# Kernel tuning notes

Measured on AMD Instinct MI355X. Metric: run time of the kernel, lower is better.

The kernel has to match this reference:

```python
import jax, jax.numpy as jnp
import numpy as np

EPS = 1e-6


def gaussian_filt(x, k, sigma):
    # x: [B,H,W,C]; depthwise gaussian conv with reflect padding, matching
    # TCFormer guassian_filt (kernel uses analytic 1/(2*pi*var) normalization).
    C = x.shape[-1]
    coords = jnp.arange(k, dtype=x.dtype)
    mean = (k - 1) / 2.0
    var = float(sigma) ** 2
    g1 = jnp.exp(-(coords - mean) ** 2 / (2.0 * var))
    gk = (g1[:, None] * g1[None, :]) / (2.0 * np.pi * var)  # [k,k]
    w = jnp.tile(gk[:, :, None, None], (1, 1, 1, C))  # HWIO, depthwise
    pad = (k - 1) // 2
    xp = jnp.pad(x, ((0, 0), (pad, pad), (pad, pad), (0, 0)), mode='reflect')
    return jax.lax.conv_general_dilated(
        xp, w, (1, 1), 'VALID',
        dimension_numbers=('NHWC', 'HWIO', 'NHWC'), feature_group_count=C)


def token2map(x, loc, H, W, kernel_size, sigma):
    # Scatter-mean tokens x [B,N,C] at normalized locations loc [B,N,2] in [-1,1]
    # onto an HxW grid, then gaussian-splat to fill holes. Returns NHWC map.
    B, N, C = x.shape
    loc = jnp.clip(loc, -1.0, 1.0)
    px = jnp.clip(jnp.round(0.5 * (loc[..., 0] + 1.0) * W - 0.5).astype(jnp.int32), 0, W - 1)
    py = jnp.clip(jnp.round(0.5 * (loc[..., 1] + 1.0) * H - 0.5).astype(jnp.int32), 0, H - 1)
    idx = py * W + px + jnp.arange(B, dtype=jnp.int32)[:, None] * (H * W)  # [B,N]
    src = jnp.concatenate([x, jnp.ones((B, N, 1), x.dtype)], axis=-1)  # [B,N,C+1]
    out = jnp.zeros((B * H * W, C + 1), x.dtype).at[idx.reshape(-1)].add(src.reshape(-1, C + 1))
    out = out.reshape(B, H, W, C + 1)
    feat, cnt = out[..., :C], out[..., C:]
    feat = feat / (cnt + EPS)
    mask = (cnt > 0).astype(x.dtype)
    feat = feat * mask
    if kernel_size > 1:
        # reconstruct_feature: fill empty cells with gaussian-interpolated values
        y = gaussian_filt(jnp.concatenate([feat, mask], axis=-1), kernel_size, sigma)
        fi, mi = y[..., :C], y[..., C:]
        fi = fi / (mi + EPS)
        fi = fi * (mi > 0).astype(x.dtype)
        feat = feat + (1.0 - mask) * fi
    return feat  # [B,H,W,C]


def layernorm(x, g, b, eps=1e-5):
    m = jnp.mean(x, axis=-1, keepdims=True)
    v = jnp.var(x, axis=-1, keepdims=True)
    return (x - m) / jnp.sqrt(v + eps) * g + b


def setup_inputs() -> dict:
    key = jax.random.key(0)
    ks = jax.random.split(key, 8)
    B, N, C, H, W = 8, 16384, 64, 128, 128
    SR = 8
    std = 0.02
    return {
        'x': jax.random.normal(ks[0], (B, N, C), jnp.float32),
        'x_source': jax.random.normal(ks[1], (B, N, C), jnp.float32),
        'loc_source': jax.random.uniform(ks[2], (B, N, 2), jnp.float32) * 2.0 - 1.0,
        'conf_source': jax.random.normal(ks[3], (B, N, 1), jnp.float32) * 0.1,
        'q_w': jax.random.normal(ks[4], (C, C), jnp.float32) * std,
        'kv_w': jax.random.normal(ks[5], (2 * C, C), jnp.float32) * std,
        'sr_w': jax.random.normal(ks[6], (SR, SR, C, C), jnp.float32) * np.sqrt(2.0 / (SR * SR * C)),
        'sr_b': jnp.zeros((C,), jnp.float32),
        'norm_w': jnp.ones((C,), jnp.float32),
        'norm_b': jnp.zeros((C,), jnp.float32),
        'proj_w': jax.random.normal(ks[7], (C, C), jnp.float32) * std,
        'proj_b': jnp.zeros((C,), jnp.float32),
        'H': H,
        'W': W,
    }


def reference(x, x_source, loc_source, conf_source, q_w, kv_w, sr_w, sr_b,
              norm_w, norm_b, proj_w, proj_b, H, W):
    B, N, C = x.shape
    num_heads = 1  # PVT stage-1
    hd = C // num_heads
    scale = hd ** -0.5
    sr = sr_w.shape[0]  # sr_ratio = 8

    # q projection: [B, nh, N, hd]
    q = (x @ q_w.T).reshape(B, N, num_heads, hd).transpose(0, 2, 1, 3)

    # token2map scatter-splat (kernel = sr_ratio + 1, sigma = 2)
    feat = token2map(x_source, loc_source, H, W, sr + 1, 2.0)  # [B,H,W,C]

    # SR conv (k = stride = sr_ratio), then layernorm
    xs = jax.lax.conv_general_dilated(
        feat, sr_w, (sr, sr), 'VALID',
        dimension_numbers=('NHWC', 'HWIO', 'NHWC')) + sr_b
    h, w = H // sr, W // sr
    xs = layernorm(xs.reshape(B, h * w, C), norm_w, norm_b)  # [B,M,C]

    # confidence map on the reduced grid (kernel_size=1 => pure scatter-mean)
    conf = token2map(conf_source, loc_source, h, w, 1, 1.0).reshape(B, h * w)  # [B,M]

    kv = (xs @ kv_w.T).reshape(B, h * w, 2, num_heads, hd)
    k = kv[:, :, 0].transpose(0, 2, 1, 3)  # [B,nh,M,hd]
    v = kv[:, :, 1].transpose(0, 2, 1, 3)

    attn = jnp.einsum('bhnd,bhmd->bhnm', q, k) * scale
    attn = attn + conf[:, None, None, :]  # additive confidence bias
    attn = jax.nn.softmax(attn, axis=-1)
    out = jnp.einsum('bhnm,bhmd->bhnd', attn, v)
    out = out.transpose(0, 2, 1, 3).reshape(B, N, C)
    return out @ proj_w.T + proj_b
```

## Files before the change

### kernel.cpp

```cpp
#include <hip/hip_runtime.h>
#include <hip/hip_bf16.h>

#define NN 16384
#define NC 64
#define GH 128
#define GW 128
#define GM 256

typedef __attribute__((ext_vector_type(8))) short bf16x8;
typedef __attribute__((ext_vector_type(4))) float f32x4;

static __device__ __forceinline__ int reflect128(int i){
  if (i < 0) i = -i;
  if (i > 127) i = 254 - i;
  return i;
}

static __device__ __forceinline__ ushort f2bf(float f){
  union { float f; unsigned u; } v; v.f = f;
  unsigned r = v.u + 0x7fffu + ((v.u >> 16) & 1u);
  return (ushort)(r >> 16);
}

static __device__ __forceinline__ int cell_of(float l, float S2, int hi){
  l = fminf(fmaxf(l, -1.f), 1.f);
  float u = l + 1.f;
  int p = (int)rintf(u*S2 - 0.5f);
  return min(max(p,0),hi);
}

__global__ __launch_bounds__(256) void k_scatter_feat(
    const float* __restrict__ xsrc, const float* __restrict__ loc,
    float* __restrict__ featg){
  int gid = blockIdx.x*256 + threadIdx.x;
  int t = gid >> 6;
  int b = t >> 14;
  int px = cell_of(loc[2*t],   64.f, 127);
  int py = cell_of(loc[2*t+1], 64.f, 127);
  int cell = (b*GH + py)*GW + px;
  atomicAdd(&featg[cell*NC + (gid & 63)], xsrc[gid]);
}

__global__ __launch_bounds__(256) void k_scatter_aux(
    const float* __restrict__ loc, const float* __restrict__ csrc,
    float* __restrict__ cnt, float* __restrict__ csum, float* __restrict__ ccnt){
  int t = blockIdx.x*256 + threadIdx.x;
  int b = t >> 14;
  int px = cell_of(loc[2*t],   64.f, 127);
  int py = cell_of(loc[2*t+1], 64.f, 127);
  atomicAdd(&cnt[(b*GH+py)*GW+px], 1.0f);
  int qx = cell_of(loc[2*t],   8.f, 15);
  int qy = cell_of(loc[2*t+1], 8.f, 15);
  int cell = b*GM + qy*16 + qx;
  atomicAdd(&csum[cell], csrc[t]);
  atomicAdd(&ccnt[cell], 1.0f);
}

__global__ __launch_bounds__(256) void k_finalize_feat(
    float* __restrict__ featg, const float* __restrict__ cnt){
  int gid = blockIdx.x*256 + threadIdx.x;
  float cn = cnt[gid>>6];
  float v  = featg[gid];
  featg[gid] = (cn > 0.f) ? v/(cn+1e-6f) : 0.f;
}

__global__ __launch_bounds__(256) void k_finalize_conf(
    const float* __restrict__ csum, const float* __restrict__ ccnt,
    float* __restrict__ conf){
  int i = blockIdx.x*256 + threadIdx.x;
  float cn = ccnt[i];
  conf[i] = (cn > 0.f) ? csum[i]/(cn+1e-6f) : 0.f;
}

__global__ __launch_bounds__(256) void k_fill2(
    const float* __restrict__ cnt, float* __restrict__ feat){
  int gid = blockIdx.x*256 + threadIdx.x;
  int p = gid >> 2, cg = gid & 3;
  if (cnt[p] > 0.f) return;
  int b = p>>14, py=(p>>7)&127, px=p&127;
  const float fn = 0.039788735772973836f;
  float g1[9];
  #pragma unroll
  for (int i=0;i<9;++i){ float d=(float)i-4.f; g1[i]=__expf(-d*d*0.125f); }
  float4 acc[4];
  #pragma unroll
  for (int i=0;i<4;++i) acc[i]=make_float4(0.f,0.f,0.f,0.f);
  float msum=0.f;
  for (int dy=0; dy<9; ++dy){
    int iy = reflect128(py-4+dy);
    for (int dx=0; dx<9; ++dx){
      int ix = reflect128(px-4+dx);
      int q  = (b*GH+iy)*GW+ix;
      if (cnt[q] <= 0.f) continue;
      float wn = g1[dy]*g1[dx]*fn;
      msum += wn;
      const float4* fr = (const float4*)&feat[q*NC + cg*16];
      #pragma unroll
      for (int k=0;k<4;++k){
        float4 vv = fr[k];
        acc[k].x += wn*vv.x; acc[k].y += wn*vv.y;
        acc[k].z += wn*vv.z; acc[k].w += wn*vv.w;
      }
    }
  }
  if (msum <= 0.f) return;
  float inv = 1.f/(msum + 1e-6f);
  float4* o = (float4*)&feat[p*NC + cg*16];
  #pragma unroll
  for (int k=0;k<4;++k)
    o[k] = make_float4(acc[k].x*inv, acc[k].y*inv, acc[k].z*inv, acc[k].w*inv);
}

static __device__ __forceinline__ int rowswz(int bid){
  return ((bid & 7) << 7) + (bid >> 3);
}

__global__ __launch_bounds__(256) void k_finfillh(
    float* __restrict__ feat, const float* __restrict__ cnt,
    float* __restrict__ feath, float* __restrict__ maskh){
  __shared__ float F[GW*NC];
  __shared__ float CR[GW];
  int py = rowswz(blockIdx.x), t = threadIdx.x;
  const float fn = 0.039788735772973836f;
  float g1n[9];
  #pragma unroll
  for (int i=0;i<9;++i){ float d=(float)i-4.f; g1n[i]=__expf(-d*d*0.125f)*fn; }
  if (t < GW) CR[t] = cnt[py*GW + t];
  __syncthreads();
  for (int i=t*4; i<GW*NC; i+=1024){
    int px = i>>6;
    float cn = CR[px];
    float inv = (cn > 0.f) ? 1.f/(cn+1e-6f) : 0.f;
    float4 v = *(const float4*)&feat[(size_t)py*GW*NC + i];
    v.x*=inv; v.y*=inv; v.z*=inv; v.w*=inv;
    *(float4*)&F[i] = v;
    *(float4*)&feat[(size_t)py*GW*NC + i] = v;
  }
  __syncthreads();
  for (int i=t*4; i<GW*NC; i+=1024){
    int px = i>>6, c = i&63;
    float4 acc = make_float4(0.f,0.f,0.f,0.f);
    #pragma unroll
    for (int dx=0; dx<9; ++dx){
      int ix = reflect128(px-4+dx);
      float w = g1n[dx];
      float4 v = *(const float4*)&F[ix*NC + c];
      acc.x += w*v.x; acc.y += w*v.y; acc.z += w*v.z; acc.w += w*v.w;
    }
    *(float4*)&feath[(size_t)py*GW*NC + i] = acc;
  }
  if (t < GW){
    float hm = 0.f;
    #pragma unroll
    for (int dx=0; dx<9; ++dx){
      int ix = reflect128(t-4+dx);
      hm += g1n[dx]*((CR[ix] > 0.f) ? 1.f : 0.f);
    }
    maskh[py*GW + t] = hm;
  }
}

__global__ __launch_bounds__(256) void k_fillv(
    float* __restrict__ feat, const float* __restrict__ cnt,
    const float* __restrict__ feath, const float* __restrict__ maskh){
  int pyg = rowswz(blockIdx.x), t = threadIdx.x;
  int b = pyg >> 7, pyl = pyg & 127;
  int px = t>>1, c0 = (t&1)<<5;
  float g1[9];
  #pragma unroll
  for (int i=0;i<9;++i){ float d=(float)i-4.f; g1[i]=__expf(-d*d*0.125f); }
  float cn = cnt[pyg*GW + px];
  float ym = 0.f;
  int ry[9];
  #pragma unroll
  for (int dy=0; dy<9; ++dy){
    ry[dy] = b*GH + reflect128(pyl-4+dy);
    ym += g1[dy]*maskh[ry[dy]*GW + px];
  }
  if (cn > 0.f || ym <= 0.f) return;
  float inv = 1.f/(ym + 1e-6f);
  float4 acc[8];
  #pragma unroll
  for (int k=0;k<8;++k) acc[k]=make_float4(0.f,0.f,0.f,0.f);
  #pragma unroll
  for (int dy=0; dy<9; ++dy){
    float w = g1[dy];
    const float4* hf = (const float4*)&feath[((size_t)ry[dy]*GW+px)*NC + c0];
    #pragma unroll
    for (int k=0;k<8;++k){
      float4 v = hf[k];
      acc[k].x += w*v.x; acc[k].y += w*v.y; acc[k].z += w*v.z; acc[k].w += w*v.w;
    }
  }
  float4* o = (float4*)&feat[((size_t)pyg*GW+px)*NC + c0];
  #pragma unroll
  for (int k=0;k<8;++k)
    o[k] = make_float4(acc[k].x*inv, acc[k].y*inv, acc[k].z*inv, acc[k].w*inv);
}

__global__ __launch_bounds__(256) void k_srconv(
    const float* __restrict__ feat, const float* __restrict__ srw,
    float* __restrict__ xs0){
  alignas(16) __shared__ float A[64*65];
  alignas(16) __shared__ float Bs[64*64];
  int mt = blockIdx.x, kh = blockIdx.y;
  int t = threadIdx.x;
  int tm = t>>4, tn = t&15;
  float acc[4][4] = {{0.f}};
  for (int kc=0; kc<8; ++kc){
    __syncthreads();
    for (int idx=t; idx<4096; idx+=256){
      int mr = idx>>6, kk = idx&63;
      int m = mt*64+mr;
      int b = m>>8, oh=(m>>4)&15, ow=m&15;
      A[mr*65+kk] = feat[(((b*GH)+(oh*8+kh))*GW + ow*8)*NC + kc*64 + kk];
    }
    for (int idx=t; idx<4096; idx+=256)
      Bs[idx] = srw[(kh*512 + kc*64)*64 + idx];
    __syncthreads();
    for (int kk=0; kk<64; ++kk){
      float4 bv = *(const float4*)&Bs[kk*64 + tn*4];
      #pragma unroll
      for (int i=0;i<4;++i){
        float av = A[(tm*4+i)*65 + kk];
        acc[i][0] += av*bv.x; acc[i][1] += av*bv.y;
        acc[i][2] += av*bv.z; acc[i][3] += av*bv.w;
      }
    }
  }
  #pragma unroll
  for (int i=0;i<4;++i)
    #pragma unroll
    for (int j=0;j<4;++j)
      atomicAdd(&xs0[(mt*64+tm*4+i)*64 + tn*4+j], acc[i][j]);
}

__global__ __launch_bounds__(256) void k_srconv2(
    const float* __restrict__ feat, const float* __restrict__ srw,
    float* __restrict__ part){
  alignas(16) __shared__ float A[64*65];
  alignas(16) __shared__ float Bs[64*64];
  int mt = blockIdx.x, kh = blockIdx.y, kq = blockIdx.z;
  int t = threadIdx.x;
  int tm = t>>4, tn = t&15;
  float acc[4][4] = {{0.f}};
  for (int kc=0; kc<4; ++kc){
    int kw = kq*4 + kc;
    __syncthreads();
    for (int idx=t; idx<4096; idx+=256){
      int mr = idx>>6, kk = idx&63;
      int m = mt*64+mr;
      int b = m>>8, oh=(m>>4)&15, ow=m&15;
      A[mr*65+kk] = feat[(((b*GH)+(oh*8+kh))*GW + ow*8 + kw)*NC + kk];
    }
    for (int idx=t; idx<4096; idx+=256)
      Bs[idx] = srw[(kh*512 + kw*64)*64 + idx];
    __syncthreads();
    for (int kk=0; kk<64; ++kk){
      float4 bv = *(const float4*)&Bs[kk*64 + tn*4];
      #pragma unroll
      for (int i=0;i<4;++i){
        float av = A[(tm*4+i)*65 + kk];
        acc[i][0] += av*bv.x; acc[i][1] += av*bv.y;
        acc[i][2] += av*bv.z; acc[i][3] += av*bv.w;
      }
    }
  }
  float* pdst = part + (size_t)(kh*2+kq)*2048*64;
  #pragma unroll
  for (int i=0;i<4;++i)
    #pragma unroll
    for (int j=0;j<4;++j)
      pdst[(mt*64+tm*4+i)*64 + tn*4+j] = acc[i][j];
}

__global__ __launch_bounds__(256) void k_ln(
    const float* __restrict__ xs0, const float* __restrict__ srb,
    const float* __restrict__ nw, const float* __restrict__ nbv,
    float* __restrict__ xs){
  int row  = blockIdx.x*4 + (threadIdx.x>>6);
  int lane = threadIdx.x & 63;
  float v = xs0[row*64+lane] + srb[lane];
  float s = v;
  #pragma unroll
  for (int off=32; off; off>>=1) s += __shfl_xor(s, off, 64);
  float mean = s*(1.f/64.f);
  float d = v - mean;
  float s2 = d*d;
  #pragma unroll
  for (int off=32; off; off>>=1) s2 += __shfl_xor(s2, off, 64);
  float var = s2*(1.f/64.f);
  xs[row*64+lane] = d*(1.f/sqrtf(var+1e-5f))*nw[lane] + nbv[lane];
}

__global__ __launch_bounds__(256) void k_ln16(
    const float* __restrict__ part, const float* __restrict__ srb,
    const float* __restrict__ nw, const float* __restrict__ nbv,
    float* __restrict__ xs){
  int row  = blockIdx.x*4 + (threadIdx.x>>6);
  int lane = threadIdx.x & 63;
  float v = srb[lane];
  #pragma unroll
  for (int ps=0; ps<16; ++ps)
    v += part[(size_t)ps*2048*64 + row*64 + lane];
  float s = v;
  #pragma unroll
  for (int off=32; off; off>>=1) s += __shfl_xor(s, off, 64);
  float mean = s*(1.f/64.f);
  float d = v - mean;
  float s2 = d*d;
  #pragma unroll
  for (int off=32; off; off>>=1) s2 += __shfl_xor(s2, off, 64);
  float var = s2*(1.f/64.f);
  xs[row*64+lane] = d*(1.f/sqrtf(var+1e-5f))*nw[lane] + nbv[lane];
}

__global__ __launch_bounds__(256) void k_kv1(
    const float* __restrict__ xs, const float* __restrict__ kvw,
    float* __restrict__ kraw, float* __restrict__ vraw){
  int gid = blockIdx.x*256 + threadIdx.x;
  int r = gid >> 6, d = gid & 63;
  const float* xr = &xs[r*64];
  float ka=0.f, va=0.f;
  for (int c=0;c<64;++c){
    float xc = xr[c];
    ka += xc*kvw[d*64+c];
    va += xc*kvw[(64+d)*64+c];
  }
  kraw[gid] = ka;
  vraw[gid] = va;
}

__global__ __launch_bounds__(256) void k_kvproj2(
    const float* __restrict__ kraw, const float* __restrict__ vraw,
    const float* __restrict__ qw, const float* __restrict__ pw,
    ushort* __restrict__ KB, ushort* __restrict__ VB){
  int gid = blockIdx.x*256 + threadIdx.x;
  int r = gid >> 6, c = gid & 63;
  int b = r >> 8, m = r & 255;
  const float* kr = &kraw[r*64];
  const float* vr = &vraw[r*64];
  float ak=0.f, av=0.f;
  for (int i=0;i<64;++i){
    ak += kr[i]*qw[i*64+c];
    av += vr[i]*pw[c*64+i];
  }
  {
    int nt = m>>4, l15 = m&15, kb = c>>5, h = (c>>3)&3, j = c&7;
    KB[((((b*16 + nt)*2 + kb)*4 + h)*16 + l15)*8 + j] = f2bf(ak);
  }
  {
    int ct = c>>4, n15 = c&15, kb2 = m>>5, h2 = (m>>3)&3, j2 = m&7;
    VB[((((b*4 + ct)*8 + kb2)*4 + h2)*16 + n15)*8 + j2] = f2bf(av);
  }
}

__global__ __launch_bounds__(256) void k_attn5(
    const float* __restrict__ x, const ushort* __restrict__ KB,
    const ushort* __restrict__ VB, const float* __restrict__ conf,
    const float* __restrict__ projb, float* __restrict__ out){
  alignas(16) __shared__ ushort P[4*4096];
  int t = threadIdx.x, w = t>>6, l = t&63;
  int b = blockIdx.x >> 8;
  int row0 = ((blockIdx.x & 255) << 6) + (w<<4);
  int l15 = l & 15, h = l >> 4;
  const ushort* KBb = KB + b*16384;
  const ushort* VBb = VB + b*16384;

  bf16x8 xa[2];
  {
    const float* xr = x + (size_t)(b*NN + row0 + l15)*64 + h*8;
    #pragma unroll
    for (int kb=0; kb<2; ++kb){
      float4 a0 = *(const float4*)(xr + 32*kb);
      float4 a1 = *(const float4*)(xr + 32*kb + 4);
      bf16x8 v;
      v[0]=(short)f2bf(a0.x); v[1]=(short)f2bf(a0.y);
      v[2]=(short)f2bf(a0.z); v[3]=(short)f2bf(a0.w);
      v[4]=(short)f2bf(a1.x); v[5]=(short)f2bf(a1.y);
      v[6]=(short)f2bf(a1.z); v[7]=(short)f2bf(a1.w);
      xa[kb]=v;
    }
  }

  f32x4 acc[16];
  #pragma unroll
  for (int nt=0;nt<16;++nt) acc[nt] = (f32x4){0.f,0.f,0.f,0.f};
  #pragma unroll
  for (int nt=0;nt<16;++nt){
    bf16x8 b0 = *(const bf16x8*)(KBb + (nt*2+0)*512 + l*8);
    bf16x8 b1 = *(const bf16x8*)(KBb + (nt*2+1)*512 + l*8);
    acc[nt] = __builtin_amdgcn_mfma_f32_16x16x32_bf16(xa[0], b0, acc[nt], 0,0,0);
    acc[nt] = __builtin_amdgcn_mfma_f32_16x16x32_bf16(xa[1], b1, acc[nt], 0,0,0);
  }

  float rs[4] = {0.f,0.f,0.f,0.f};
  ushort* Pw = P + w*4096;
  #pragma unroll
  for (int nt=0;nt<16;++nt){
    float cf = conf[b*GM + nt*16 + l15];
    #pragma unroll
    for (int reg=0;reg<4;++reg){
      float p = __expf(fmaf(acc[nt][reg], 0.125f, cf));
      rs[reg] += p;
      int m   = nt*16 + l15;
      int row = h*4 + reg;
      int ld  = ((m>>3)&3)*16 + row;
      int idx = ((m>>5)*512 + ld*8 + (m&7)) ^ (ld & 0x38);
      Pw[idx] = f2bf(p);
    }
  }
  #pragma unroll
  for (int off=1; off<16; off<<=1){
    #pragma unroll
    for (int reg=0;reg<4;++reg) rs[reg] += __shfl_xor(rs[reg], off, 64);
  }

  f32x4 oacc[4];
  #pragma unroll
  for (int ct=0;ct<4;++ct) oacc[ct] = (f32x4){0.f,0.f,0.f,0.f};
  #pragma unroll
  for (int kb2=0;kb2<8;++kb2){
    int ridx = (kb2*512 + l*8) ^ (l & 0x38);
    bf16x8 pa = *(const bf16x8*)(Pw + ridx);
    #pragma unroll
    for (int ct=0;ct<4;++ct){
      bf16x8 vb = *(const bf16x8*)(VBb + (ct*8+kb2)*512 + l*8);
      oacc[ct] = __builtin_amdgcn_mfma_f32_16x16x32_bf16(pa, vb, oacc[ct], 0,0,0);
    }
  }

  float* OT = (float*)Pw;
  #pragma unroll
  for (int ct=0;ct<4;++ct){
    float pb4 = projb[ct*16 + l15];
    #pragma unroll
    for (int reg=0;reg<4;++reg)
      OT[(h*4+reg)*68 + ct*16 + l15] = oacc[ct][reg]/rs[reg] + pb4;
  }
  #pragma unroll
  for (int i=0;i<4;++i){
    int row = i*4 + h;
    float4 v = *(const float4*)&OT[row*68 + l15*4];
    *(float4*)&out[(size_t)(b*NN + row0 + row)*64 + l15*4] = v;
  }
}

extern "C" void kernel_launch(void* const* d_in, const int* in_sizes, int n_in,
                              void* d_out, int out_size, void* d_ws, size_t ws_size,
                              hipStream_t stream){
  const float* x    = (const float*)d_in[0];
  const float* xsrc = (const float*)d_in[1];
  const float* loc  = (const float*)d_in[2];
  const float* csrc = (const float*)d_in[3];
  const float* qw   = (const float*)d_in[4];
  const float* kvw  = (const float*)d_in[5];
  const float* srw  = (const float*)d_in[6];
  const float* srb  = (const float*)d_in[7];
  const float* nw   = (const float*)d_in[8];
  const float* nbv  = (const float*)d_in[9];
  const float* pw   = (const float*)d_in[10];
  const float* pb   = (const float*)d_in[11];
  float* out = (float*)d_out;
  float* ws = (float*)d_ws;

  size_t of_feat  = 0;
  size_t of_cnt   = of_feat  + 8ull*GH*GW*NC;
  size_t of_csum  = of_cnt   + 8ull*GH*GW;
  size_t of_ccnt  = of_csum  + 8ull*GM;
  size_t zero_end = of_ccnt  + 8ull*GM;
  size_t of_feath = zero_end;
  size_t of_maskh = of_feath + 8ull*GH*GW*NC;
  size_t of_part  = of_maskh + 8ull*GH*GW;
  size_t of_conf  = of_part  + 16ull*2048*64;
  size_t of_xs    = of_conf  + 8ull*GM;
  size_t of_kr    = of_xs    + 8ull*GM*NC;
  size_t of_vr    = of_kr    + 8ull*GM*NC;
  size_t of_kb    = of_vr    + 8ull*GM*NC;
  size_t of_vb    = of_kb    + 8ull*8192;
  size_t total_p  = of_vb    + 8ull*8192;

  if (ws_size >= total_p*sizeof(float)){
    hipMemsetAsync(ws, 0, zero_end*sizeof(float), stream);
    k_scatter_feat <<<8*NN*NC/256, 256, 0, stream>>>(xsrc, loc, ws+of_feat);
    k_scatter_aux  <<<8*NN/256,    256, 0, stream>>>(loc, csrc, ws+of_cnt, ws+of_csum, ws+of_ccnt);
    k_finalize_conf<<<8*GM/256,    256, 0, stream>>>(ws+of_csum, ws+of_ccnt, ws+of_conf);
    k_finfillh     <<<8*GH,        256, 0, stream>>>(ws+of_feat, ws+of_cnt, ws+of_feath, ws+of_maskh);
    k_fillv        <<<8*GH,        256, 0, stream>>>(ws+of_feat, ws+of_cnt, ws+of_feath, ws+of_maskh);
    dim3 gconv(32, 8, 2);
    k_srconv2      <<<gconv,       256, 0, stream>>>(ws+of_feat, srw, ws+of_part);
    k_ln16         <<<8*GM/4,      256, 0, stream>>>(ws+of_part, srb, nw, nbv, ws+of_xs);
    k_kv1          <<<8*GM*NC/256, 256, 0, stream>>>(ws+of_xs, kvw, ws+of_kr, ws+of_vr);
    k_kvproj2      <<<8*GM*NC/256, 256, 0, stream>>>(ws+of_kr, ws+of_vr, qw, pw,
                                                     (ushort*)(ws+of_kb), (ushort*)(ws+of_vb));
    k_attn5        <<<8*NN/64,     256, 0, stream>>>(x, (const ushort*)(ws+of_kb),
                                                     (const ushort*)(ws+of_vb),
                                                     ws+of_conf, pb, out);
  } else {
    size_t f_feat = 0;
    size_t f_cnt  = f_feat + 8ull*GH*GW*NC;
    size_t f_csum = f_cnt  + 8ull*GH*GW;
    size_t f_ccnt = f_csum + 8ull*GM;
    size_t f_xs0  = f_ccnt + 8ull*GM;
    size_t f_zero = f_xs0  + 8ull*GM*NC;
    size_t f_conf = f_zero;
    size_t f_xs   = f_conf + 8ull*GM;
    size_t f_kr   = f_xs   + 8ull*GM*NC;
    size_t f_vr   = f_kr   + 8ull*GM*NC;
    size_t f_kb   = f_vr   + 8ull*GM*NC;
    size_t f_vb   = f_kb   + 8ull*8192;
    hipMemsetAsync(ws, 0, f_zero*sizeof(float), stream);
    k_scatter_feat <<<8*NN*NC/256, 256, 0, stream>>>(xsrc, loc, ws+f_feat);
    k_scatter_aux  <<<8*NN/256,    256, 0, stream>>>(loc, csrc, ws+f_cnt, ws+f_csum, ws+f_ccnt);
    k_finalize_feat<<<8*GH*GW*NC/256, 256, 0, stream>>>(ws+f_feat, ws+f_cnt);
    k_finalize_conf<<<8*GM/256,    256, 0, stream>>>(ws+f_csum, ws+f_ccnt, ws+f_conf);
    k_fill2        <<<8*GH*GW*4/256, 256, 0, stream>>>(ws+f_cnt, ws+f_feat);
    dim3 gconv(8*GM/64, 8);
    k_srconv       <<<gconv,       256, 0, stream>>>(ws+f_feat, srw, ws+f_xs0);
    k_ln           <<<8*GM/4,      256, 0, stream>>>(ws+f_xs0, srb, nw, nbv, ws+f_xs);
    k_kv1          <<<8*GM*NC/256, 256, 0, stream>>>(ws+f_xs, kvw, ws+f_kr, ws+f_vr);
    k_kvproj2      <<<8*GM*NC/256, 256, 0, stream>>>(ws+f_kr, ws+f_vr, qw, pw,
                                                     (ushort*)(ws+f_kb), (ushort*)(ws+f_vb));
    k_attn5        <<<8*NN/64,     256, 0, stream>>>(x, (const ushort*)(ws+f_kb),
                                                     (const ushort*)(ws+f_vb),
                                                     ws+f_conf, pb, out);
  }
}
```

Measured before the change: 206.6 us.

## Fuse layernorm and KV projections into one kernel; chunk attention softmax-PV loop

```diff
diff --git a/kernel.cpp b/kernel.cpp
--- a/kernel.cpp
+++ b/kernel.cpp
@@ -293,28 +293,6 @@
   xs[row*64+lane] = d*(1.f/sqrtf(var+1e-5f))*nw[lane] + nbv[lane];
 }
 
-__global__ __launch_bounds__(256) void k_ln16(
-    const float* __restrict__ part, const float* __restrict__ srb,
-    const float* __restrict__ nw, const float* __restrict__ nbv,
-    float* __restrict__ xs){
-  int row  = blockIdx.x*4 + (threadIdx.x>>6);
-  int lane = threadIdx.x & 63;
-  float v = srb[lane];
-  #pragma unroll
-  for (int ps=0; ps<16; ++ps)
-    v += part[(size_t)ps*2048*64 + row*64 + lane];
-  float s = v;
-  #pragma unroll
-  for (int off=32; off; off>>=1) s += __shfl_xor(s, off, 64);
-  float mean = s*(1.f/64.f);
-  float d = v - mean;
-  float s2 = d*d;
-  #pragma unroll
-  for (int off=32; off; off>>=1) s2 += __shfl_xor(s2, off, 64);
-  float var = s2*(1.f/64.f);
-  xs[row*64+lane] = d*(1.f/sqrtf(var+1e-5f))*nw[lane] + nbv[lane];
-}
-
 __global__ __launch_bounds__(256) void k_kv1(
     const float* __restrict__ xs, const float* __restrict__ kvw,
     float* __restrict__ kraw, float* __restrict__ vraw){
@@ -355,6 +333,56 @@
   }
 }
 
+__global__ __launch_bounds__(256) void k_kvfused(
+    const float* __restrict__ part, const float* __restrict__ srb,
+    const float* __restrict__ nw, const float* __restrict__ nbv,
+    const float* __restrict__ kvw, const float* __restrict__ qw,
+    const float* __restrict__ pw,
+    ushort* __restrict__ KB, ushort* __restrict__ VB){
+  __shared__ float XR[4][64], KR[4][64], VR[4][64];
+  int t = threadIdx.x;
+  int rl = t>>6, d = t&63;
+  int r  = blockIdx.x*4 + rl;
+  float v = srb[d];
+  #pragma unroll
+  for (int ps=0; ps<16; ++ps)
+    v += part[(size_t)ps*2048*64 + r*64 + d];
+  float s = v;
+  #pragma unroll
+  for (int off=32; off; off>>=1) s += __shfl_xor(s, off, 64);
+  float mean = s*(1.f/64.f);
+  float dd = v - mean;
+  float s2 = dd*dd;
+  #pragma unroll
+  for (int off=32; off; off>>=1) s2 += __shfl_xor(s2, off, 64);
+  float var = s2*(1.f/64.f);
+  XR[rl][d] = dd*(1.f/sqrtf(var+1e-5f))*nw[d] + nbv[d];
+  __syncthreads();
+  float ka=0.f, va=0.f;
+  for (int cc=0; cc<64; ++cc){
+    float xc = XR[rl][cc];
+    ka += xc*kvw[d*64+cc];
+    va += xc*kvw[(64+d)*64+cc];
+  }
+  KR[rl][d] = ka; VR[rl][d] = va;
+  __syncthreads();
+  int c = d;
+  float ak=0.f, av=0.f;
+  for (int i=0;i<64;++i){
+    ak += KR[rl][i]*qw[i*64+c];
+    av += VR[rl][i]*pw[c*64+i];
+  }
+  int b = r>>8, m = r&255;
+  {
+    int nt = m>>4, l15 = m&15, kb = c>>5, h = (c>>3)&3, j = c&7;
+    KB[((((b*16 + nt)*2 + kb)*4 + h)*16 + l15)*8 + j] = f2bf(ak);
+  }
+  {
+    int ct = c>>4, n15 = c&15, kb2 = m>>5, h2 = (m>>3)&3, j2 = m&7;
+    VB[((((b*4 + ct)*8 + kb2)*4 + h2)*16 + n15)*8 + j2] = f2bf(av);
+  }
+}
+
 __global__ __launch_bounds__(256) void k_attn5(
     const float* __restrict__ x, const ushort* __restrict__ KB,
     const ushort* __restrict__ VB, const float* __restrict__ conf,
@@ -366,7 +394,6 @@
   int l15 = l & 15, h = l >> 4;
   const ushort* KBb = KB + b*16384;
   const ushort* VBb = VB + b*16384;
-
   bf16x8 xa[2];
   {
     const float* xr = x + (size_t)(b*NN + row0 + l15)*64 + h*8;
@@ -382,7 +409,6 @@
       xa[kb]=v;
     }
   }
-
   f32x4 acc[16];
   #pragma unroll
   for (int nt=0;nt<16;++nt) acc[nt] = (f32x4){0.f,0.f,0.f,0.f};
@@ -393,7 +419,6 @@
     acc[nt] = __builtin_amdgcn_mfma_f32_16x16x32_bf16(xa[0], b0, acc[nt], 0,0,0);
     acc[nt] = __builtin_amdgcn_mfma_f32_16x16x32_bf16(xa[1], b1, acc[nt], 0,0,0);
   }
-
   float rs[4] = {0.f,0.f,0.f,0.f};
   ushort* Pw = P + w*4096;
   #pragma unroll
@@ -415,7 +440,6 @@
     #pragma unroll
     for (int reg=0;reg<4;++reg) rs[reg] += __shfl_xor(rs[reg], off, 64);
   }
-
   f32x4 oacc[4];
   #pragma unroll
   for (int ct=0;ct<4;++ct) oacc[ct] = (f32x4){0.f,0.f,0.f,0.f};
@@ -428,6 +452,102 @@
       bf16x8 vb = *(const bf16x8*)(VBb + (ct*8+kb2)*512 + l*8);
       oacc[ct] = __builtin_amdgcn_mfma_f32_16x16x32_bf16(pa, vb, oacc[ct], 0,0,0);
     }
+  }
+  float* OT = (float*)Pw;
+  #pragma unroll
+  for (int ct=0;ct<4;++ct){
+    float pb4 = projb[ct*16 + l15];
+    #pragma unroll
+    for (int reg=0;reg<4;++reg)
+      OT[(h*4+reg)*68 + ct*16 + l15] = oacc[ct][reg]/rs[reg] + pb4;
+  }
+  #pragma unroll
+  for (int i=0;i<4;++i){
+    int row = i*4 + h;
+    float4 v = *(const float4*)&OT[row*68 + l15*4];
+    *(float4*)&out[(size_t)(b*NN + row0 + row)*64 + l15*4] = v;
+  }
+}
+
+__global__ __launch_bounds__(256) void k_attn6(
+    const float* __restrict__ x, const ushort* __restrict__ KB,
+    const ushort* __restrict__ VB, const float* __restrict__ conf,
+    const float* __restrict__ projb, float* __restrict__ out){
+  alignas(16) __shared__ ushort P[4*4096];
+  int t = threadIdx.x, w = t>>6, l = t&63;
+  int b = blockIdx.x >> 8;
+  int row0 = ((blockIdx.x & 255) << 6) + (w<<4);
+  int l15 = l & 15, h = l >> 4;
+  const ushort* KBb = KB + b*16384;
+  const ushort* VBb = VB + b*16384;
+
+  bf16x8 xa[2];
+  {
+    const float* xr = x + (size_t)(b*NN + row0 + l15)*64 + h*8;
+    #pragma unroll
+    for (int kb=0; kb<2; ++kb){
+      float4 a0 = *(const float4*)(xr + 32*kb);
+      float4 a1 = *(const float4*)(xr + 32*kb + 4);
+      bf16x8 v;
+      v[0]=(short)f2bf(a0.x); v[1]=(short)f2bf(a0.y);
+      v[2]=(short)f2bf(a0.z); v[3]=(short)f2bf(a0.w);
+      v[4]=(short)f2bf(a1.x); v[5]=(short)f2bf(a1.y);
+      v[6]=(short)f2bf(a1.z); v[7]=(short)f2bf(a1.w);
+      xa[kb]=v;
+    }
+  }
+
+  float rs[4] = {0.f,0.f,0.f,0.f};
+  f32x4 oacc[4];
+  #pragma unroll
+  for (int ct=0;ct<4;++ct) oacc[ct] = (f32x4){0.f,0.f,0.f,0.f};
+  ushort* Pw = P + w*4096;
+
+  #pragma unroll
+  for (int c=0;c<4;++c){
+    f32x4 acc[4];
+    #pragma unroll
+    for (int q=0;q<4;++q) acc[q] = (f32x4){0.f,0.f,0.f,0.f};
+    #pragma unroll
+    for (int q=0;q<4;++q){
+      int nt = c*4 + q;
+      bf16x8 b0 = *(const bf16x8*)(KBb + (nt*2+0)*512 + l*8);
+      bf16x8 b1 = *(const bf16x8*)(KBb + (nt*2+1)*512 + l*8);
+      acc[q] = __builtin_amdgcn_mfma_f32_16x16x32_bf16(xa[0], b0, acc[q], 0,0,0);
+      acc[q] = __builtin_amdgcn_mfma_f32_16x16x32_bf16(xa[1], b1, acc[q], 0,0,0);
+    }
+    #pragma unroll
+    for (int q=0;q<4;++q){
+      int nt = c*4 + q;
+      float cf = conf[b*GM + nt*16 + l15];
+      #pragma unroll
+      for (int reg=0;reg<4;++reg){
+        float p = __expf(fmaf(acc[q][reg], 0.125f, cf));
+        rs[reg] += p;
+        int m   = nt*16 + l15;
+        int row = h*4 + reg;
+        int ld  = ((m>>3)&3)*16 + row;
+        int idx = ((m>>5)*512 + ld*8 + (m&7)) ^ (ld & 0x38);
+        Pw[idx] = f2bf(p);
+      }
+    }
+    #pragma unroll
+    for (int kk=0;kk<2;++kk){
+      int kb2 = c*2 + kk;
+      int ridx = (kb2*512 + l*8) ^ (l & 0x38);
+      bf16x8 pa = *(const bf16x8*)(Pw + ridx);
+      #pragma unroll
+      for (int ct=0;ct<4;++ct){
+        bf16x8 vb = *(const bf16x8*)(VBb + (ct*8+kb2)*512 + l*8);
+        oacc[ct] = __builtin_amdgcn_mfma_f32_16x16x32_bf16(pa, vb, oacc[ct], 0,0,0);
+      }
+    }
+  }
+
+  #pragma unroll
+  for (int off=1; off<16; off<<=1){
+    #pragma unroll
+    for (int reg=0;reg<4;++reg) rs[reg] += __shfl_xor(rs[reg], off, 64);
   }
 
   float* OT = (float*)Pw;
@@ -473,10 +593,7 @@
   size_t of_maskh = of_feath + 8ull*GH*GW*NC;
   size_t of_part  = of_maskh + 8ull*GH*GW;
   size_t of_conf  = of_part  + 16ull*2048*64;
-  size_t of_xs    = of_conf  + 8ull*GM;
-  size_t of_kr    = of_xs    + 8ull*GM*NC;
-  size_t of_vr    = of_kr    + 8ull*GM*NC;
-  size_t of_kb    = of_vr    + 8ull*GM*NC;
+  size_t of_kb    = of_conf  + 8ull*GM;
   size_t of_vb    = of_kb    + 8ull*8192;
   size_t total_p  = of_vb    + 8ull*8192;
 
@@ -489,11 +606,9 @@
     k_fillv        <<<8*GH,        256, 0, stream>>>(ws+of_feat, ws+of_cnt, ws+of_feath, ws+of_maskh);
     dim3 gconv(32, 8, 2);
     k_srconv2      <<<gconv,       256, 0, stream>>>(ws+of_feat, srw, ws+of_part);
-    k_ln16         <<<8*GM/4,      256, 0, stream>>>(ws+of_part, srb, nw, nbv, ws+of_xs);
-    k_kv1          <<<8*GM*NC/256, 256, 0, stream>>>(ws+of_xs, kvw, ws+of_kr, ws+of_vr);
-    k_kvproj2      <<<8*GM*NC/256, 256, 0, stream>>>(ws+of_kr, ws+of_vr, qw, pw,
+    k_kvfused      <<<8*GM/4,      256, 0, stream>>>(ws+of_part, srb, nw, nbv, kvw, qw, pw,
                                                      (ushort*)(ws+of_kb), (ushort*)(ws+of_vb));
-    k_attn5        <<<8*NN/64,     256, 0, stream>>>(x, (const ushort*)(ws+of_kb),
+    k_attn6        <<<8*NN/64,     256, 0, stream>>>(x, (const ushort*)(ws+of_kb),
                                                      (const ushort*)(ws+of_vb),
                                                      ws+of_conf, pb, out);
   } else {
```

After: 187.0 us. 9.4% less time.
